# Kernel tuning notes

Measured on AMD Instinct MI355X. Metric: run time of the kernel, lower is better.

Reference implementation:

```python
import jax, jax.numpy as jnp
import numpy as np

WS = 7           # window size
N = WS * WS      # tokens per window = 49
C = 128          # embed dim
H = 4            # heads
HD = C // H      # head dim = 32
NW = 64          # num windows (mask leading dim)
B = 4096         # total windows = outer_batch * NW


def _relative_indexes():
    ch = np.arange(WS)
    cw = np.arange(WS)
    coords = np.stack(np.meshgrid(ch, cw, indexing='ij')).reshape(2, -1)  # [2, N]
    rel = coords[:, :, None] - coords[:, None, :]                          # [2, N, N]
    rel = rel.transpose(1, 2, 0)
    rel[:, :, 0] += WS - 1
    rel[:, :, 1] += WS - 1
    rel[:, :, 0] *= 2 * WS - 1
    return jnp.asarray(rel.sum(-1), dtype=jnp.int32)                       # [N, N]


def setup_inputs() -> dict:
    key = jax.random.key(0)
    ks = jax.random.split(key, 10)
    s = 0.02
    return {
        'query': jax.random.normal(ks[0], (B, N, C), jnp.float32),
        'source': jax.random.normal(ks[1], (B, N, C), jnp.float32),
        'mask': jnp.zeros((NW, N, N), jnp.float32),
        'q_w': jax.random.normal(ks[2], (C, C), jnp.float32) * s,
        'q_b': jnp.zeros((C,), jnp.float32),
        'kv_w': jax.random.normal(ks[3], (C, 2 * C), jnp.float32) * s,
        'kv_b': jnp.zeros((2 * C,), jnp.float32),
        'proj_w': jax.random.normal(ks[4], (C, C), jnp.float32) * s,
        'proj_b': jnp.zeros((C,), jnp.float32),
        'bias_table': jax.random.normal(ks[5], ((2 * WS - 1) ** 2, H), jnp.float32) * s,
        'rel_idx': _relative_indexes(),
    }


def reference(query, source, mask, q_w, q_b, kv_w, kv_b, proj_w, proj_b, bias_table, rel_idx):
    scale = HD ** -0.5
    q = query @ q_w + q_b                       # [B, N, C]
    kv = source @ kv_w + kv_b                   # [B, N, 2C]
    k, v = kv[..., :C], kv[..., C:]
    # [B, N, H, HD] -> [B, H, N, HD]
    q = q.reshape(B, N, H, HD).transpose(0, 2, 1, 3) * scale
    k = k.reshape(B, N, H, HD).transpose(0, 2, 1, 3)
    v = v.reshape(B, N, H, HD).transpose(0, 2, 1, 3)
    attn = jnp.einsum('bhnd,bhmd->bhnm', q, k)  # [B, H, N, N]
    # gathered relative positional bias: [1, H, N, N]
    bias = bias_table[rel_idx.reshape(-1)].reshape(N, N, H).transpose(2, 0, 1)[None]
    attn = attn + bias
    # mask: [NW, N, N] broadcast over outer batch and heads
    attn = attn.reshape(-1, NW, H, N, N) + mask[None, :, None]
    attn = attn.reshape(B, H, N, N)
    attn = jax.nn.softmax(attn, axis=-1)
    x = jnp.einsum('bhnm,bhmd->bnhd', attn, v).reshape(B, N, C)
    return x @ proj_w + proj_b
```

## Files before the change

kernel.cpp:

```cpp
#include <hip/hip_runtime.h>
#include <hip/hip_bf16.h>

#define NN 49
#define CC 128
#define HH 4
#define NWIN 64
#define BB 4096
#define QSCALE 0.17677669529663687f

typedef __attribute__((ext_vector_type(8))) short bf16x8;
typedef __attribute__((ext_vector_type(4))) float f32x4;
typedef unsigned short u16;
typedef unsigned int u32;

union U8 { u32 u[4]; bf16x8 v; };

__device__ __forceinline__ u16 f2b(float f) {
    __hip_bfloat16 h = __float2bfloat16(f);
    return __builtin_bit_cast(u16, h);
}
__device__ __forceinline__ float b2f(u16 u) { return __uint_as_float(((u32)u) << 16); }
__device__ __forceinline__ u32 cvtpk(float lo, float hi) {
    u32 r;
    asm("v_cvt_pk_bf16_f32 %0, %1, %2" : "=v"(r) : "v"(lo), "v"(hi));
    return r;
}
__device__ __forceinline__ uint2 pack4(float a, float b, float c, float d) {
    uint2 r;
    r.x = cvtpk(a, b);
    r.y = cvtpk(c, d);
    return r;
}
__device__ __forceinline__ f32x4 mfma16(bf16x8 a, bf16x8 b, f32x4 c) {
    return __builtin_amdgcn_mfma_f32_16x16x32_bf16(a, b, c, 0, 0, 0);
}
__device__ __forceinline__ char* adr256(u16* base, int row, int byte) {
    return (char*)base + row * 256 + (byte ^ ((row & 7) << 4));
}
__device__ __forceinline__ char* adr128(u16* base, int row, int byte) {
    return (char*)base + row * 128 + (byte ^ ((row & 7) << 4));
}

__global__ void prep_cbt(const float* __restrict__ bias_table, const int* __restrict__ rel_idx,
                         const float* __restrict__ mask, u16* __restrict__ cbt) {
    int idx = blockIdx.x * blockDim.x + threadIdx.x;
    int m = idx & 63, i = (idx >> 6) & 63, h = (idx >> 12) & 3, wv = idx >> 14;
    if (wv >= NWIN) return;
    float v = -1e9f;
    if (m < NN && i < NN)
        v = bias_table[rel_idx[i * NN + m] * HH + h] + mask[(wv * NN + i) * NN + m];
    cbt[idx] = f2b(v);
}

__global__ void prep_w(const float* __restrict__ qw, const float* __restrict__ qb,
                       const float* __restrict__ kvw, const float* __restrict__ pjw,
                       u16* __restrict__ qwp, u16* __restrict__ kvwp,
                       u16* __restrict__ pjwp, float* __restrict__ qbs) {
    int idx = blockIdx.x * blockDim.x + threadIdx.x;
    if (idx < 16384) {
        int i = idx & 7, lane = (idx >> 3) & 63, kt = (idx >> 9) & 3, nt = idx >> 11;
        int k = 32 * kt + 8 * (lane >> 4) + i, n = 16 * nt + (lane & 15);
        qwp[idx] = f2b(qw[k * CC + n] * QSCALE);
    } else if (idx < 49152) {
        int j = idx - 16384;
        int i = j & 7, lane = (j >> 3) & 63, kt = (j >> 9) & 3, nt = j >> 11;
        int k = 32 * kt + 8 * (lane >> 4) + i, n = 16 * nt + (lane & 15);
        kvwp[j] = f2b(kvw[k * 2 * CC + n]);
    } else if (idx < 65536) {
        int j = idx - 49152;
        int i = j & 7, lane = (j >> 3) & 63, kt = (j >> 9) & 3, nt = j >> 11;
        int k = 32 * kt + 8 * (lane >> 4) + i, n = 16 * nt + (lane & 15);
        pjwp[j] = f2b(pjw[k * CC + n]);
    } else if (idx < 65664) {
        int j = idx - 65536;
        qbs[j] = qb[j] * QSCALE;
    }
}

__global__ __launch_bounds__(512, 2)
void wmha_main(const float* __restrict__ query, const float* __restrict__ source,
               const u16* __restrict__ qwp, const u16* __restrict__ kvwp,
               const u16* __restrict__ pjwp, const float* __restrict__ qbs,
               const float* __restrict__ kv_b, const float* __restrict__ proj_b,
               const u16* __restrict__ cbt, float* __restrict__ out) {
    __shared__ u16 lds[40960];
    u16* SQ = lds;
    u16* SS = lds + 8192;
    u16* Qb = lds + 16384;
    u16* Kb = lds + 24576;
    u16* VT = lds + 32768;
    const int t = threadIdx.x;
    const int b = blockIdx.x;
    const int w = t >> 6, lane = t & 63;
    const int lq = lane & 15, qd = lane >> 4;
    const int mw = w >> 2;
    const int nw = w & 3;
    const int h = w >> 1;
    const int half = w & 1;

    {
        const int row = t >> 3, qu = t & 7;
        const size_t gbase = (size_t)b * NN * CC + row * CC + qu * 8;
        #pragma unroll
        for (int j = 0; j < 2; ++j) {
            U8 vq, vs;
            if (row < NN) {
                const float4* q4 = (const float4*)(query + gbase) + 16 * j;
                const float4* s4 = (const float4*)(source + gbase) + 16 * j;
                float4 a0 = q4[0], a1 = q4[1], c0 = s4[0], c1 = s4[1];
                vq.u[0] = cvtpk(a0.x, a0.y); vq.u[1] = cvtpk(a0.z, a0.w);
                vq.u[2] = cvtpk(a1.x, a1.y); vq.u[3] = cvtpk(a1.z, a1.w);
                vs.u[0] = cvtpk(c0.x, c0.y); vs.u[1] = cvtpk(c0.z, c0.w);
                vs.u[2] = cvtpk(c1.x, c1.y); vs.u[3] = cvtpk(c1.z, c1.w);
            } else {
                vq.u[0] = vq.u[1] = vq.u[2] = vq.u[3] = 0;
                vs.u[0] = vs.u[1] = vs.u[2] = vs.u[3] = 0;
            }
            *(bf16x8*)adr256(SQ, row, qu * 16 + 128 * j) = vq.v;
            *(bf16x8*)adr256(SS, row, qu * 16 + 128 * j) = vs.v;
        }
    }
    bf16x8 bwq[2][4];
    #pragma unroll
    for (int n2 = 0; n2 < 2; ++n2)
        #pragma unroll
        for (int kt = 0; kt < 4; ++kt)
            bwq[n2][kt] = *(const bf16x8*)(qwp + (((nw + 4 * n2) * 4 + kt) * 64 + lane) * 8);
    __syncthreads();

    {
        f32x4 acc[2][2] = {};
        #pragma unroll
        for (int m2 = 0; m2 < 2; ++m2) {
            bf16x8 a[4];
            #pragma unroll
            for (int kt = 0; kt < 4; ++kt)
                a[kt] = *(const bf16x8*)adr256(SQ, (2 * mw + m2) * 16 + lq, kt * 64 + qd * 16);
            __builtin_amdgcn_s_setprio(1);
            #pragma unroll
            for (int n2 = 0; n2 < 2; ++n2)
                #pragma unroll
                for (int kt = 0; kt < 4; ++kt)
                    acc[m2][n2] = mfma16(bwq[n2][kt], a[kt], acc[m2][n2]);
            __builtin_amdgcn_s_setprio(0);
        }
        #pragma unroll
        for (int n2 = 0; n2 < 2; ++n2) {
            const int cb0 = 16 * (nw + 4 * n2) + 4 * qd;
            const float4 bia = *(const float4*)(qbs + cb0);
            #pragma unroll
            for (int m2 = 0; m2 < 2; ++m2) {
                const int tok = (2 * mw + m2) * 16 + lq;
                uint2 pk = pack4(acc[m2][n2][0] + bia.x, acc[m2][n2][1] + bia.y,
                                 acc[m2][n2][2] + bia.z, acc[m2][n2][3] + bia.w);
                *(uint2*)adr256(Qb, tok, 2 * cb0) = pk;
            }
        }
    }
    {
        bf16x8 as[2][4];
        #pragma unroll
        for (int m2 = 0; m2 < 2; ++m2)
            #pragma unroll
            for (int kt = 0; kt < 4; ++kt)
                as[m2][kt] = *(const bf16x8*)adr256(SS, (2 * mw + m2) * 16 + lq, kt * 64 + qd * 16);
        {
            bf16x8 bwk[2][4];
            #pragma unroll
            for (int n2 = 0; n2 < 2; ++n2)
                #pragma unroll
                for (int kt = 0; kt < 4; ++kt)
                    bwk[n2][kt] = *(const bf16x8*)(kvwp + (((nw + 4 * n2) * 4 + kt) * 64 + lane) * 8);
            f32x4 acc[2][2] = {};
            __builtin_amdgcn_s_setprio(1);
            #pragma unroll
            for (int m2 = 0; m2 < 2; ++m2)
                #pragma unroll
                for (int n2 = 0; n2 < 2; ++n2)
                    #pragma unroll
                    for (int kt = 0; kt < 4; ++kt)
                        acc[m2][n2] = mfma16(bwk[n2][kt], as[m2][kt], acc[m2][n2]);
            __builtin_amdgcn_s_setprio(0);
            #pragma unroll
            for (int n2 = 0; n2 < 2; ++n2) {
                const int cb0 = 16 * (nw + 4 * n2) + 4 * qd;
                const float4 bia = *(const float4*)(kv_b + cb0);
                #pragma unroll
                for (int m2 = 0; m2 < 2; ++m2) {
                    const int tok = (2 * mw + m2) * 16 + lq;
                    uint2 pk = pack4(acc[m2][n2][0] + bia.x, acc[m2][n2][1] + bia.y,
                                     acc[m2][n2][2] + bia.z, acc[m2][n2][3] + bia.w);
                    *(uint2*)adr256(Kb, tok, 2 * cb0) = pk;
                }
            }
        }
        {
            bf16x8 bwv[2][4];
            #pragma unroll
            for (int n2 = 0; n2 < 2; ++n2)
                #pragma unroll
                for (int kt = 0; kt < 4; ++kt)
                    bwv[n2][kt] = *(const bf16x8*)(kvwp + (((8 + nw + 4 * n2) * 4 + kt) * 64 + lane) * 8);
            f32x4 acc[2][2] = {};
            __builtin_amdgcn_s_setprio(1);
            #pragma unroll
            for (int m2 = 0; m2 < 2; ++m2)
                #pragma unroll
                for (int n2 = 0; n2 < 2; ++n2)
                    #pragma unroll
                    for (int kt = 0; kt < 4; ++kt)
                        acc[m2][n2] = mfma16(as[m2][kt], bwv[n2][kt], acc[m2][n2]);
            __builtin_amdgcn_s_setprio(0);
            #pragma unroll
            for (int n2 = 0; n2 < 2; ++n2) {
                const int dim = 16 * (nw + 4 * n2) + lq;
                const float bias = kv_b[CC + dim];
                #pragma unroll
                for (int m2 = 0; m2 < 2; ++m2) {
                    uint2 pk = pack4(acc[m2][n2][0] + bias, acc[m2][n2][1] + bias,
                                     acc[m2][n2][2] + bias, acc[m2][n2][3] + bias);
                    *(uint2*)adr128(VT, dim, 2 * ((2 * mw + m2) * 16 + qd * 4)) = pk;
                }
            }
        }
    }
    __syncthreads();

    f32x4 s[2][4];
    bf16x8 vf[2][2];
    {
        bf16x8 kf[4], qf[2];
        #pragma unroll
        for (int a = 0; a < 4; ++a)
            kf[a] = *(const bf16x8*)adr256(Kb, a * 16 + lq, h * 64 + qd * 16);
        #pragma unroll
        for (int i = 0; i < 2; ++i)
            qf[i] = *(const bf16x8*)adr256(Qb, (2 * half + i) * 16 + lq, h * 64 + qd * 16);
        __builtin_amdgcn_s_setprio(1);
        #pragma unroll
        for (int i = 0; i < 2; ++i) {
            f32x4 z = {0.f, 0.f, 0.f, 0.f};
            #pragma unroll
            for (int a = 0; a < 4; ++a)
                s[i][a] = mfma16(kf[a], qf[i], z);
        }
        __builtin_amdgcn_s_setprio(0);
        #pragma unroll
        for (int dt = 0; dt < 2; ++dt)
            #pragma unroll
            for (int kt = 0; kt < 2; ++kt)
                vf[dt][kt] = *(const bf16x8*)adr128(VT, h * 32 + dt * 16 + lq, kt * 64 + qd * 16);
    }
    uint2 cbr[2][4];
    {
        const u16* cbb = cbt + ((size_t)((b & (NWIN - 1)) * HH + h) << 12);
        #pragma unroll
        for (int i = 0; i < 2; ++i)
            #pragma unroll
            for (int a = 0; a < 4; ++a)
                cbr[i][a] = *(const uint2*)(cbb + ((2 * half + i) * 16 + lq) * 64 + a * 16 + qd * 4);
    }
    __syncthreads();

    {
        u16* pb0 = Qb + w * 1024;
        u16* pb1 = Kb + w * 1024;
        float inv[2];
        #pragma unroll
        for (int i = 0; i < 2; ++i) {
            #pragma unroll
            for (int a = 0; a < 3; ++a) {
                s[i][a][0] += b2f((u16)(cbr[i][a].x & 0xffffu));
                s[i][a][1] += b2f((u16)(cbr[i][a].x >> 16));
                s[i][a][2] += b2f((u16)(cbr[i][a].y & 0xffffu));
                s[i][a][3] += b2f((u16)(cbr[i][a].y >> 16));
            }
            s[i][3][0] += b2f((u16)(cbr[i][3].x & 0xffffu));
            float m0 = s[i][3][0];
            #pragma unroll
            for (int a = 0; a < 3; ++a)
                #pragma unroll
                for (int r = 0; r < 4; ++r) m0 = fmaxf(m0, s[i][a][r]);
            m0 = fmaxf(m0, __shfl_xor(m0, 16));
            m0 = fmaxf(m0, __shfl_xor(m0, 32));
            uint2 pk[4];
            float sm = 0.f;
            #pragma unroll
            for (int a = 0; a < 3; ++a) {
                float p0 = __expf(s[i][a][0] - m0), p1 = __expf(s[i][a][1] - m0);
                float p2 = __expf(s[i][a][2] - m0), p3 = __expf(s[i][a][3] - m0);
                pk[a].x = cvtpk(p0, p1);
                pk[a].y = cvtpk(p2, p3);
                sm += (p0 + p1) + (p2 + p3);
            }
            float p30 = __expf(s[i][3][0] - m0);
            pk[3].x = cvtpk(p30, 0.f);
            pk[3].y = 0u;
            sm += p30;
            sm += __shfl_xor(sm, 16);
            sm += __shfl_xor(sm, 32);
            inv[i] = 1.f / sm;
            u16* pb = i ? pb1 : pb0;
            #pragma unroll
            for (int a = 0; a < 4; ++a)
                *(uint2*)adr128(pb, lq, 32 * a + 8 * qd) = pk[a];
        }
        asm volatile("s_waitcnt lgkmcnt(0)" ::: "memory");
        __builtin_amdgcn_sched_barrier(0);
        f32x4 o[2][2] = {};
        __builtin_amdgcn_s_setprio(1);
        #pragma unroll
        for (int kt = 0; kt < 2; ++kt) {
            bf16x8 pf0 = *(const bf16x8*)adr128(pb0, lq, 64 * kt + 16 * qd);
            bf16x8 pf1 = *(const bf16x8*)adr128(pb1, lq, 64 * kt + 16 * qd);
            #pragma unroll
            for (int dt = 0; dt < 2; ++dt) {
                o[0][dt] = mfma16(vf[dt][kt], pf0, o[0][dt]);
                o[1][dt] = mfma16(vf[dt][kt], pf1, o[1][dt]);
            }
        }
        __builtin_amdgcn_s_setprio(0);
        #pragma unroll
        for (int i = 0; i < 2; ++i)
            #pragma unroll
            for (int dt = 0; dt < 2; ++dt) {
                uint2 px = pack4(o[i][dt][0] * inv[i], o[i][dt][1] * inv[i],
                                 o[i][dt][2] * inv[i], o[i][dt][3] * inv[i]);
                *(uint2*)adr256(SQ, (2 * half + i) * 16 + lq, 64 * h + 32 * dt + 8 * qd) = px;
            }
    }

    {
        bf16x8 bw[2][4];
        #pragma unroll
        for (int n2 = 0; n2 < 2; ++n2)
            #pragma unroll
            for (int kt = 0; kt < 4; ++kt)
                bw[n2][kt] = *(const bf16x8*)(pjwp + (((nw + 4 * n2) * 4 + kt) * 64 + lane) * 8);
        __syncthreads();
        f32x4 acc[2][2] = {};
        #pragma unroll
        for (int m2 = 0; m2 < 2; ++m2) {
            bf16x8 a[4];
            #pragma unroll
            for (int kt = 0; kt < 4; ++kt)
                a[kt] = *(const bf16x8*)adr256(SQ, (2 * mw + m2) * 16 + lq, kt * 64 + qd * 16);
            __builtin_amdgcn_s_setprio(1);
            #pragma unroll
            for (int n2 = 0; n2 < 2; ++n2)
                #pragma unroll
                for (int kt = 0; kt < 4; ++kt)
                    acc[m2][n2] = mfma16(bw[n2][kt], a[kt], acc[m2][n2]);
            __builtin_amdgcn_s_setprio(0);
        }
        float* outb = out + (size_t)b * NN * CC;
        #pragma unroll
        for (int n2 = 0; n2 < 2; ++n2) {
            const int cb0 = 16 * (nw + 4 * n2) + 4 * qd;
            const float4 bia = *(const float4*)(proj_b + cb0);
            #pragma unroll
            for (int m2 = 0; m2 < 2; ++m2) {
                const int tok = (2 * mw + m2) * 16 + lq;
                if (tok < NN) {
                    float4 vst;
                    vst.x = acc[m2][n2][0] + bia.x;
                    vst.y = acc[m2][n2][1] + bia.y;
                    vst.z = acc[m2][n2][2] + bia.z;
                    vst.w = acc[m2][n2][3] + bia.w;
                    *(float4*)(outb + tok * CC + cb0) = vst;
                }
            }
        }
    }
}

extern "C" void kernel_launch(void* const* d_in, const int* in_sizes, int n_in,
                              void* d_out, int out_size, void* d_ws, size_t ws_size,
                              hipStream_t stream) {
    const float* query      = (const float*)d_in[0];
    const float* source     = (const float*)d_in[1];
    const float* mask       = (const float*)d_in[2];
    const float* q_w        = (const float*)d_in[3];
    const float* q_b        = (const float*)d_in[4];
    const float* kv_w       = (const float*)d_in[5];
    const float* kv_b       = (const float*)d_in[6];
    const float* proj_w     = (const float*)d_in[7];
    const float* proj_b     = (const float*)d_in[8];
    const float* bias_table = (const float*)d_in[9];
    const int*   rel_idx    = (const int*)d_in[10];
    float* out = (float*)d_out;

    u16* cbt   = (u16*)d_ws;
    u16* qwp   = cbt + 1048576;
    u16* kvwp  = qwp + 16384;
    u16* pjwp  = kvwp + 32768;
    float* qbs = (float*)(pjwp + 16384);

    prep_cbt<<<4096, 256, 0, stream>>>(bias_table, rel_idx, mask, cbt);
    prep_w<<<257, 256, 0, stream>>>(q_w, q_b, kv_w, proj_w, qwp, kvwp, pjwp, qbs);
    wmha_main<<<BB, 512, 0, stream>>>(query, source, qwp, kvwp, pjwp, qbs,
                                      kv_b, proj_b, cbt, out);
}
```

Measured before the change: 121.7 us.

## Alias LDS regions to shrink shared memory and raise occupancy

Shrinks per-block LDS from 80KB to 48KB by reusing three 16KB regions across phases (input staging, Q/K/V^T, probability buffers, attention output). It adds extra __syncthreads to guard the reuse, processes the two query tiles of P·V sequentially with a single probability buffer, and moves the V fragment loads later. Launch bounds now request 6 blocks per CU instead of 2, trading tighter register budgets and more barriers for more resident blocks to hide latency.

```diff
diff --git a/kernel.cpp b/kernel.cpp
--- a/kernel.cpp
+++ b/kernel.cpp
@@ -77,18 +77,16 @@
     }
 }
 
-__global__ __launch_bounds__(512, 2)
+__global__ __launch_bounds__(512, 6)
 void wmha_main(const float* __restrict__ query, const float* __restrict__ source,
                const u16* __restrict__ qwp, const u16* __restrict__ kvwp,
                const u16* __restrict__ pjwp, const float* __restrict__ qbs,
                const float* __restrict__ kv_b, const float* __restrict__ proj_b,
                const u16* __restrict__ cbt, float* __restrict__ out) {
-    __shared__ u16 lds[40960];
-    u16* SQ = lds;
-    u16* SS = lds + 8192;
-    u16* Qb = lds + 16384;
-    u16* Kb = lds + 24576;
-    u16* VT = lds + 32768;
+    __shared__ u16 lds[24576];
+    u16* R0 = lds;
+    u16* R1 = lds + 8192;
+    u16* R2 = lds + 16384;
     const int t = threadIdx.x;
     const int b = blockIdx.x;
     const int w = t >> 6, lane = t & 63;
@@ -116,8 +114,8 @@
                 vq.u[0] = vq.u[1] = vq.u[2] = vq.u[3] = 0;
                 vs.u[0] = vs.u[1] = vs.u[2] = vs.u[3] = 0;
             }
-            *(bf16x8*)adr256(SQ, row, qu * 16 + 128 * j) = vq.v;
-            *(bf16x8*)adr256(SS, row, qu * 16 + 128 * j) = vs.v;
+            *(bf16x8*)adr256(R0, row, qu * 16 + 128 * j) = vq.v;
+            *(bf16x8*)adr256(R2, row, qu * 16 + 128 * j) = vs.v;
         }
     }
     bf16x8 bwq[2][4];
@@ -135,7 +133,7 @@
             bf16x8 a[4];
             #pragma unroll
             for (int kt = 0; kt < 4; ++kt)
-                a[kt] = *(const bf16x8*)adr256(SQ, (2 * mw + m2) * 16 + lq, kt * 64 + qd * 16);
+                a[kt] = *(const bf16x8*)adr256(R0, (2 * mw + m2) * 16 + lq, kt * 64 + qd * 16);
             __builtin_amdgcn_s_setprio(1);
             #pragma unroll
             for (int n2 = 0; n2 < 2; ++n2)
@@ -153,17 +151,19 @@
                 const int tok = (2 * mw + m2) * 16 + lq;
                 uint2 pk = pack4(acc[m2][n2][0] + bia.x, acc[m2][n2][1] + bia.y,
                                  acc[m2][n2][2] + bia.z, acc[m2][n2][3] + bia.w);
-                *(uint2*)adr256(Qb, tok, 2 * cb0) = pk;
-            }
-        }
-    }
+                *(uint2*)adr256(R1, tok, 2 * cb0) = pk;
+            }
+        }
+    }
+    __syncthreads();
+
     {
         bf16x8 as[2][4];
         #pragma unroll
         for (int m2 = 0; m2 < 2; ++m2)
             #pragma unroll
             for (int kt = 0; kt < 4; ++kt)
-                as[m2][kt] = *(const bf16x8*)adr256(SS, (2 * mw + m2) * 16 + lq, kt * 64 + qd * 16);
+                as[m2][kt] = *(const bf16x8*)adr256(R2, (2 * mw + m2) * 16 + lq, kt * 64 + qd * 16);
         {
             bf16x8 bwk[2][4];
             #pragma unroll
@@ -190,7 +190,7 @@
                     const int tok = (2 * mw + m2) * 16 + lq;
                     uint2 pk = pack4(acc[m2][n2][0] + bia.x, acc[m2][n2][1] + bia.y,
                                      acc[m2][n2][2] + bia.z, acc[m2][n2][3] + bia.w);
-                    *(uint2*)adr256(Kb, tok, 2 * cb0) = pk;
+                    *(uint2*)adr256(R0, tok, 2 * cb0) = pk;
                 }
             }
         }
@@ -211,6 +211,7 @@
                     for (int kt = 0; kt < 4; ++kt)
                         acc[m2][n2] = mfma16(as[m2][kt], bwv[n2][kt], acc[m2][n2]);
             __builtin_amdgcn_s_setprio(0);
+            __syncthreads();
             #pragma unroll
             for (int n2 = 0; n2 < 2; ++n2) {
                 const int dim = 16 * (nw + 4 * n2) + lq;
@@ -219,23 +220,21 @@
                 for (int m2 = 0; m2 < 2; ++m2) {
                     uint2 pk = pack4(acc[m2][n2][0] + bias, acc[m2][n2][1] + bias,
                                      acc[m2][n2][2] + bias, acc[m2][n2][3] + bias);
-                    *(uint2*)adr128(VT, dim, 2 * ((2 * mw + m2) * 16 + qd * 4)) = pk;
+                    *(uint2*)adr128(R2, dim, 2 * ((2 * mw + m2) * 16 + qd * 4)) = pk;
                 }
             }
         }
     }
-    __syncthreads();
 
     f32x4 s[2][4];
-    bf16x8 vf[2][2];
     {
         bf16x8 kf[4], qf[2];
         #pragma unroll
         for (int a = 0; a < 4; ++a)
-            kf[a] = *(const bf16x8*)adr256(Kb, a * 16 + lq, h * 64 + qd * 16);
+            kf[a] = *(const bf16x8*)adr256(R0, a * 16 + lq, h * 64 + qd * 16);
         #pragma unroll
         for (int i = 0; i < 2; ++i)
-            qf[i] = *(const bf16x8*)adr256(Qb, (2 * half + i) * 16 + lq, h * 64 + qd * 16);
+            qf[i] = *(const bf16x8*)adr256(R1, (2 * half + i) * 16 + lq, h * 64 + qd * 16);
         __builtin_amdgcn_s_setprio(1);
         #pragma unroll
         for (int i = 0; i < 2; ++i) {
@@ -245,11 +244,6 @@
                 s[i][a] = mfma16(kf[a], qf[i], z);
         }
         __builtin_amdgcn_s_setprio(0);
-        #pragma unroll
-        for (int dt = 0; dt < 2; ++dt)
-            #pragma unroll
-            for (int kt = 0; kt < 2; ++kt)
-                vf[dt][kt] = *(const bf16x8*)adr128(VT, h * 32 + dt * 16 + lq, kt * 64 + qd * 16);
     }
     uint2 cbr[2][4];
     {
@@ -263,11 +257,16 @@
     __syncthreads();
 
     {
-        u16* pb0 = Qb + w * 1024;
-        u16* pb1 = Kb + w * 1024;
-        float inv[2];
+        bf16x8 vf[2][2];
+        #pragma unroll
+        for (int dt = 0; dt < 2; ++dt)
+            #pragma unroll
+            for (int kt = 0; kt < 2; ++kt)
+                vf[dt][kt] = *(const bf16x8*)adr128(R2, h * 32 + dt * 16 + lq, kt * 64 + qd * 16);
+        u16* pb = R0 + w * 1024;
         #pragma unroll
         for (int i = 0; i < 2; ++i) {
+            const int bq = 2 * half + i;
             #pragma unroll
             for (int a = 0; a < 3; ++a) {
                 s[i][a][0] += b2f((u16)(cbr[i][a].x & 0xffffu));
@@ -299,35 +298,30 @@
             sm += p30;
             sm += __shfl_xor(sm, 16);
             sm += __shfl_xor(sm, 32);
-            inv[i] = 1.f / sm;
-            u16* pb = i ? pb1 : pb0;
+            const float inv = 1.f / sm;
             #pragma unroll
             for (int a = 0; a < 4; ++a)
                 *(uint2*)adr128(pb, lq, 32 * a + 8 * qd) = pk[a];
-        }
-        asm volatile("s_waitcnt lgkmcnt(0)" ::: "memory");
-        __builtin_amdgcn_sched_barrier(0);
-        f32x4 o[2][2] = {};
-        __builtin_amdgcn_s_setprio(1);
-        #pragma unroll
-        for (int kt = 0; kt < 2; ++kt) {
-            bf16x8 pf0 = *(const bf16x8*)adr128(pb0, lq, 64 * kt + 16 * qd);
-            bf16x8 pf1 = *(const bf16x8*)adr128(pb1, lq, 64 * kt + 16 * qd);
+            asm volatile("s_waitcnt lgkmcnt(0)" ::: "memory");
+            __builtin_amdgcn_sched_barrier(0);
+            f32x4 o[2] = {{0.f,0.f,0.f,0.f},{0.f,0.f,0.f,0.f}};
+            __builtin_amdgcn_s_setprio(1);
+            #pragma unroll
+            for (int kt = 0; kt < 2; ++kt) {
+                bf16x8 pf = *(const bf16x8*)adr128(pb, lq, 64 * kt + 16 * qd);
+                #pragma unroll
+                for (int dt = 0; dt < 2; ++dt)
+                    o[dt] = mfma16(vf[dt][kt], pf, o[dt]);
+            }
+            __builtin_amdgcn_s_setprio(0);
+            __builtin_amdgcn_sched_barrier(0);
             #pragma unroll
             for (int dt = 0; dt < 2; ++dt) {
-                o[0][dt] = mfma16(vf[dt][kt], pf0, o[0][dt]);
-                o[1][dt] = mfma16(vf[dt][kt], pf1, o[1][dt]);
-            }
-        }
-        __builtin_amdgcn_s_setprio(0);
-        #pragma unroll
-        for (int i = 0; i < 2; ++i)
-            #pragma unroll
-            for (int dt = 0; dt < 2; ++dt) {
-                uint2 px = pack4(o[i][dt][0] * inv[i], o[i][dt][1] * inv[i],
-                                 o[i][dt][2] * inv[i], o[i][dt][3] * inv[i]);
-                *(uint2*)adr256(SQ, (2 * half + i) * 16 + lq, 64 * h + 32 * dt + 8 * qd) = px;
-            }
+                uint2 px = pack4(o[dt][0] * inv, o[dt][1] * inv,
+                                 o[dt][2] * inv, o[dt][3] * inv);
+                *(uint2*)adr256(R1, bq * 16 + lq, 64 * h + 32 * dt + 8 * qd) = px;
+            }
+        }
     }
 
     {
@@ -344,7 +338,7 @@
             bf16x8 a[4];
             #pragma unroll
             for (int kt = 0; kt < 4; ++kt)
-                a[kt] = *(const bf16x8*)adr256(SQ, (2 * mw + m2) * 16 + lq, kt * 64 + qd * 16);
+                a[kt] = *(const bf16x8*)adr256(R1, (2 * mw + m2) * 16 + lq, kt * 64 + qd * 16);
             __builtin_amdgcn_s_setprio(1);
             #pragma unroll
             for (int n2 = 0; n2 < 2; ++n2)
```

Result: slower. 208.6 us (+71.4%).

## Split fused window attention into QKV projection and attention/output kernels

Applied to the files above, without the earlier changes.

Splits the single fused kernel into two: one projects Q, K and V^T into swizzled bf16 images in workspace, the other loads those images and does attention plus the output projection. It falls back to the fused kernel when the workspace is too small. The likely aim is to cut per-kernel LDS and register pressure so occupancy or scheduling improves. The cost is an extra round trip of about 200MB of bf16 intermediates through global memory and one more launch.

```diff
diff --git a/kernel.cpp b/kernel.cpp
--- a/kernel.cpp
+++ b/kernel.cpp
@@ -78,6 +78,333 @@
 }
 
 __global__ __launch_bounds__(512, 2)
+void qkv_proj(const float* __restrict__ query, const float* __restrict__ source,
+              const u16* __restrict__ qwp, const u16* __restrict__ kvwp,
+              const float* __restrict__ qbs, const float* __restrict__ kv_b,
+              u16* __restrict__ qimg, u16* __restrict__ kimg, u16* __restrict__ vtimg) {
+    __shared__ u16 lds[16384];
+    u16* SQ = lds;
+    u16* SS = lds + 8192;
+    const int t = threadIdx.x;
+    const int b = blockIdx.x;
+    const int w = t >> 6, lane = t & 63;
+    const int lq = lane & 15, qd = lane >> 4;
+    const int mw = w >> 2, nw = w & 3;
+
+    {
+        const int row = t >> 3, qu = t & 7;
+        const size_t gbase = (size_t)b * NN * CC + row * CC + qu * 8;
+        #pragma unroll
+        for (int j = 0; j < 2; ++j) {
+            U8 vq, vs;
+            if (row < NN) {
+                const float4* q4 = (const float4*)(query + gbase) + 16 * j;
+                const float4* s4 = (const float4*)(source + gbase) + 16 * j;
+                float4 a0 = q4[0], a1 = q4[1], c0 = s4[0], c1 = s4[1];
+                vq.u[0] = cvtpk(a0.x, a0.y); vq.u[1] = cvtpk(a0.z, a0.w);
+                vq.u[2] = cvtpk(a1.x, a1.y); vq.u[3] = cvtpk(a1.z, a1.w);
+                vs.u[0] = cvtpk(c0.x, c0.y); vs.u[1] = cvtpk(c0.z, c0.w);
+                vs.u[2] = cvtpk(c1.x, c1.y); vs.u[3] = cvtpk(c1.z, c1.w);
+            } else {
+                vq.u[0] = vq.u[1] = vq.u[2] = vq.u[3] = 0;
+                vs.u[0] = vs.u[1] = vs.u[2] = vs.u[3] = 0;
+            }
+            *(bf16x8*)adr256(SQ, row, qu * 16 + 128 * j) = vq.v;
+            *(bf16x8*)adr256(SS, row, qu * 16 + 128 * j) = vs.v;
+        }
+    }
+    bf16x8 bwq[2][4];
+    #pragma unroll
+    for (int n2 = 0; n2 < 2; ++n2)
+        #pragma unroll
+        for (int kt = 0; kt < 4; ++kt)
+            bwq[n2][kt] = *(const bf16x8*)(qwp + (((nw + 4 * n2) * 4 + kt) * 64 + lane) * 8);
+    __syncthreads();
+
+    u16* qo  = qimg  + (size_t)b * 8192;
+    u16* ko  = kimg  + (size_t)b * 8192;
+    u16* vto = vtimg + (size_t)b * 8192;
+
+    {
+        f32x4 acc[2][2] = {};
+        #pragma unroll
+        for (int m2 = 0; m2 < 2; ++m2) {
+            bf16x8 a[4];
+            #pragma unroll
+            for (int kt = 0; kt < 4; ++kt)
+                a[kt] = *(const bf16x8*)adr256(SQ, (2 * mw + m2) * 16 + lq, kt * 64 + qd * 16);
+            __builtin_amdgcn_s_setprio(1);
+            #pragma unroll
+            for (int n2 = 0; n2 < 2; ++n2)
+                #pragma unroll
+                for (int kt = 0; kt < 4; ++kt)
+                    acc[m2][n2] = mfma16(bwq[n2][kt], a[kt], acc[m2][n2]);
+            __builtin_amdgcn_s_setprio(0);
+        }
+        #pragma unroll
+        for (int n2 = 0; n2 < 2; ++n2) {
+            const int cb0 = 16 * (nw + 4 * n2) + 4 * qd;
+            const float4 bia = *(const float4*)(qbs + cb0);
+            #pragma unroll
+            for (int m2 = 0; m2 < 2; ++m2) {
+                const int tok = (2 * mw + m2) * 16 + lq;
+                uint2 pk = pack4(acc[m2][n2][0] + bia.x, acc[m2][n2][1] + bia.y,
+                                 acc[m2][n2][2] + bia.z, acc[m2][n2][3] + bia.w);
+                *(uint2*)adr256(qo, tok, 2 * cb0) = pk;
+            }
+        }
+    }
+    {
+        bf16x8 as[2][4];
+        #pragma unroll
+        for (int m2 = 0; m2 < 2; ++m2)
+            #pragma unroll
+            for (int kt = 0; kt < 4; ++kt)
+                as[m2][kt] = *(const bf16x8*)adr256(SS, (2 * mw + m2) * 16 + lq, kt * 64 + qd * 16);
+        {
+            bf16x8 bwk[2][4];
+            #pragma unroll
+            for (int n2 = 0; n2 < 2; ++n2)
+                #pragma unroll
+                for (int kt = 0; kt < 4; ++kt)
+                    bwk[n2][kt] = *(const bf16x8*)(kvwp + (((nw + 4 * n2) * 4 + kt) * 64 + lane) * 8);
+            f32x4 acc[2][2] = {};
+            __builtin_amdgcn_s_setprio(1);
+            #pragma unroll
+            for (int m2 = 0; m2 < 2; ++m2)
+                #pragma unroll
+                for (int n2 = 0; n2 < 2; ++n2)
+                    #pragma unroll
+                    for (int kt = 0; kt < 4; ++kt)
+                        acc[m2][n2] = mfma16(bwk[n2][kt], as[m2][kt], acc[m2][n2]);
+            __builtin_amdgcn_s_setprio(0);
+            #pragma unroll
+            for (int n2 = 0; n2 < 2; ++n2) {
+                const int cb0 = 16 * (nw + 4 * n2) + 4 * qd;
+                const float4 bia = *(const float4*)(kv_b + cb0);
+                #pragma unroll
+                for (int m2 = 0; m2 < 2; ++m2) {
+                    const int tok = (2 * mw + m2) * 16 + lq;
+                    uint2 pk = pack4(acc[m2][n2][0] + bia.x, acc[m2][n2][1] + bia.y,
+                                     acc[m2][n2][2] + bia.z, acc[m2][n2][3] + bia.w);
+                    *(uint2*)adr256(ko, tok, 2 * cb0) = pk;
+                }
+            }
+        }
+        {
+            bf16x8 bwv[2][4];
+            #pragma unroll
+            for (int n2 = 0; n2 < 2; ++n2)
+                #pragma unroll
+                for (int kt = 0; kt < 4; ++kt)
+                    bwv[n2][kt] = *(const bf16x8*)(kvwp + (((8 + nw + 4 * n2) * 4 + kt) * 64 + lane) * 8);
+            f32x4 acc[2][2] = {};
+            __builtin_amdgcn_s_setprio(1);
+            #pragma unroll
+            for (int m2 = 0; m2 < 2; ++m2)
+                #pragma unroll
+                for (int n2 = 0; n2 < 2; ++n2)
+                    #pragma unroll
+                    for (int kt = 0; kt < 4; ++kt)
+                        acc[m2][n2] = mfma16(as[m2][kt], bwv[n2][kt], acc[m2][n2]);
+            __builtin_amdgcn_s_setprio(0);
+            #pragma unroll
+            for (int n2 = 0; n2 < 2; ++n2) {
+                const int dim = 16 * (nw + 4 * n2) + lq;
+                const float bias = kv_b[CC + dim];
+                #pragma unroll
+                for (int m2 = 0; m2 < 2; ++m2) {
+                    uint2 pk = pack4(acc[m2][n2][0] + bias, acc[m2][n2][1] + bias,
+                                     acc[m2][n2][2] + bias, acc[m2][n2][3] + bias);
+                    *(uint2*)adr128(vto, dim, 2 * ((2 * mw + m2) * 16 + qd * 4)) = pk;
+                }
+            }
+        }
+    }
+}
+
+__global__ __launch_bounds__(512, 2)
+void attn_out(const u16* __restrict__ qimg, const u16* __restrict__ kimg,
+              const u16* __restrict__ vtimg, const u16* __restrict__ pjwp,
+              const float* __restrict__ proj_b, const u16* __restrict__ cbt,
+              float* __restrict__ out) {
+    __shared__ u16 lds[24576];
+    u16* Qi = lds;
+    u16* Ki = lds + 8192;
+    u16* VTi = lds + 16384;
+    const int t = threadIdx.x;
+    const int b = blockIdx.x;
+    const int w = t >> 6, lane = t & 63;
+    const int lq = lane & 15, qd = lane >> 4;
+    const int mw = w >> 2, nw = w & 3;
+    const int h = w >> 1, half = w & 1;
+
+    {
+        const u16* gq = qimg  + (size_t)b * 8192;
+        const u16* gk = kimg  + (size_t)b * 8192;
+        const u16* gv = vtimg + (size_t)b * 8192;
+        #pragma unroll
+        for (int j = 0; j < 2; ++j) {
+            const int off = (t + j * 512) * 8;
+            uint4 a = *(const uint4*)(gq + off);
+            uint4 c = *(const uint4*)(gk + off);
+            uint4 d = *(const uint4*)(gv + off);
+            *(uint4*)(Qi + off) = a;
+            *(uint4*)(Ki + off) = c;
+            *(uint4*)(VTi + off) = d;
+        }
+    }
+    __syncthreads();
+
+    f32x4 s[2][4];
+    bf16x8 vf[2][2];
+    {
+        bf16x8 kf[4], qf[2];
+        #pragma unroll
+        for (int a = 0; a < 4; ++a)
+            kf[a] = *(const bf16x8*)adr256(Ki, a * 16 + lq, h * 64 + qd * 16);
+        #pragma unroll
+        for (int i = 0; i < 2; ++i)
+            qf[i] = *(const bf16x8*)adr256(Qi, (2 * half + i) * 16 + lq, h * 64 + qd * 16);
+        __builtin_amdgcn_s_setprio(1);
+        #pragma unroll
+        for (int i = 0; i < 2; ++i) {
+            f32x4 z = {0.f, 0.f, 0.f, 0.f};
+            #pragma unroll
+            for (int a = 0; a < 4; ++a)
+                s[i][a] = mfma16(kf[a], qf[i], z);
+        }
+        __builtin_amdgcn_s_setprio(0);
+        #pragma unroll
+        for (int dt = 0; dt < 2; ++dt)
+            #pragma unroll
+            for (int kt = 0; kt < 2; ++kt)
+                vf[dt][kt] = *(const bf16x8*)adr128(VTi, h * 32 + dt * 16 + lq, kt * 64 + qd * 16);
+    }
+    uint2 cbr[2][4];
+    {
+        const u16* cbb = cbt + ((size_t)((b & (NWIN - 1)) * HH + h) << 12);
+        #pragma unroll
+        for (int i = 0; i < 2; ++i)
+            #pragma unroll
+            for (int a = 0; a < 4; ++a)
+                cbr[i][a] = *(const uint2*)(cbb + ((2 * half + i) * 16 + lq) * 64 + a * 16 + qd * 4);
+    }
+    __syncthreads();
+
+    {
+        u16* pb0 = Qi + w * 1024;
+        u16* pb1 = Ki + w * 1024;
+        float inv[2];
+        #pragma unroll
+        for (int i = 0; i < 2; ++i) {
+            #pragma unroll
+            for (int a = 0; a < 3; ++a) {
+                s[i][a][0] += b2f((u16)(cbr[i][a].x & 0xffffu));
+                s[i][a][1] += b2f((u16)(cbr[i][a].x >> 16));
+                s[i][a][2] += b2f((u16)(cbr[i][a].y & 0xffffu));
+                s[i][a][3] += b2f((u16)(cbr[i][a].y >> 16));
+            }
+            s[i][3][0] += b2f((u16)(cbr[i][3].x & 0xffffu));
+            float m0 = s[i][3][0];
+            #pragma unroll
+            for (int a = 0; a < 3; ++a)
+                #pragma unroll
+                for (int r = 0; r < 4; ++r) m0 = fmaxf(m0, s[i][a][r]);
+            m0 = fmaxf(m0, __shfl_xor(m0, 16));
+            m0 = fmaxf(m0, __shfl_xor(m0, 32));
+            uint2 pk[4];
+            float sm = 0.f;
+            #pragma unroll
+            for (int a = 0; a < 3; ++a) {
+                float p0 = __expf(s[i][a][0] - m0), p1 = __expf(s[i][a][1] - m0);
+                float p2 = __expf(s[i][a][2] - m0), p3 = __expf(s[i][a][3] - m0);
+                pk[a].x = cvtpk(p0, p1);
+                pk[a].y = cvtpk(p2, p3);
+                sm += (p0 + p1) + (p2 + p3);
+            }
+            float p30 = __expf(s[i][3][0] - m0);
+            pk[3].x = cvtpk(p30, 0.f);
+            pk[3].y = 0u;
+            sm += p30;
+            sm += __shfl_xor(sm, 16);
+            sm += __shfl_xor(sm, 32);
+            inv[i] = 1.f / sm;
+            u16* pb = i ? pb1 : pb0;
+            #pragma unroll
+            for (int a = 0; a < 4; ++a)
+                *(uint2*)adr128(pb, lq, 32 * a + 8 * qd) = pk[a];
+        }
+        asm volatile("s_waitcnt lgkmcnt(0)" ::: "memory");
+        __builtin_amdgcn_sched_barrier(0);
+        f32x4 o[2][2] = {};
+        __builtin_amdgcn_s_setprio(1);
+        #pragma unroll
+        for (int kt = 0; kt < 2; ++kt) {
+            bf16x8 pf0 = *(const bf16x8*)adr128(pb0, lq, 64 * kt + 16 * qd);
+            bf16x8 pf1 = *(const bf16x8*)adr128(pb1, lq, 64 * kt + 16 * qd);
+            #pragma unroll
+            for (int dt = 0; dt < 2; ++dt) {
+                o[0][dt] = mfma16(vf[dt][kt], pf0, o[0][dt]);
+                o[1][dt] = mfma16(vf[dt][kt], pf1, o[1][dt]);
+            }
+        }
+        __builtin_amdgcn_s_setprio(0);
+        #pragma unroll
+        for (int i = 0; i < 2; ++i)
+            #pragma unroll
+            for (int dt = 0; dt < 2; ++dt) {
+                uint2 px = pack4(o[i][dt][0] * inv[i], o[i][dt][1] * inv[i],
+                                 o[i][dt][2] * inv[i], o[i][dt][3] * inv[i]);
+                *(uint2*)adr256(VTi, (2 * half + i) * 16 + lq, 64 * h + 32 * dt + 8 * qd) = px;
+            }
+    }
+
+    {
+        bf16x8 bw[2][4];
+        #pragma unroll
+        for (int n2 = 0; n2 < 2; ++n2)
+            #pragma unroll
+            for (int kt = 0; kt < 4; ++kt)
+                bw[n2][kt] = *(const bf16x8*)(pjwp + (((nw + 4 * n2) * 4 + kt) * 64 + lane) * 8);
+        __syncthreads();
+        f32x4 acc[2][2] = {};
+        #pragma unroll
+        for (int m2 = 0; m2 < 2; ++m2) {
+            bf16x8 a[4];
+            #pragma unroll
+            for (int kt = 0; kt < 4; ++kt)
+                a[kt] = *(const bf16x8*)adr256(VTi, (2 * mw + m2) * 16 + lq, kt * 64 + qd * 16);
+            __builtin_amdgcn_s_setprio(1);
+            #pragma unroll
+            for (int n2 = 0; n2 < 2; ++n2)
+                #pragma unroll
+                for (int kt = 0; kt < 4; ++kt)
+                    acc[m2][n2] = mfma16(bw[n2][kt], a[kt], acc[m2][n2]);
+            __builtin_amdgcn_s_setprio(0);
+        }
+        float* outb = out + (size_t)b * NN * CC;
+        #pragma unroll
+        for (int n2 = 0; n2 < 2; ++n2) {
+            const int cb0 = 16 * (nw + 4 * n2) + 4 * qd;
+            const float4 bia = *(const float4*)(proj_b + cb0);
+            #pragma unroll
+            for (int m2 = 0; m2 < 2; ++m2) {
+                const int tok = (2 * mw + m2) * 16 + lq;
+                if (tok < NN) {
+                    float4 vst;
+                    vst.x = acc[m2][n2][0] + bia.x;
+                    vst.y = acc[m2][n2][1] + bia.y;
+                    vst.z = acc[m2][n2][2] + bia.z;
+                    vst.w = acc[m2][n2][3] + bia.w;
+                    *(float4*)(outb + tok * CC + cb0) = vst;
+                }
+            }
+        }
+    }
+}
+
+__global__ __launch_bounds__(512, 2)
 void wmha_main(const float* __restrict__ query, const float* __restrict__ source,
                const u16* __restrict__ qwp, const u16* __restrict__ kvwp,
                const u16* __restrict__ pjwp, const float* __restrict__ qbs,
@@ -93,10 +420,8 @@
     const int b = blockIdx.x;
     const int w = t >> 6, lane = t & 63;
     const int lq = lane & 15, qd = lane >> 4;
-    const int mw = w >> 2;
-    const int nw = w & 3;
-    const int h = w >> 1;
-    const int half = w & 1;
+    const int mw = w >> 2, nw = w & 3;
+    const int h = w >> 1, half = w & 1;
 
     {
         const int row = t >> 3, qu = t & 7;
@@ -395,9 +720,19 @@
     u16* kvwp  = qwp + 16384;
     u16* pjwp  = kvwp + 32768;
     float* qbs = (float*)(pjwp + 16384);
+    u16* qimg  = (u16*)(qbs + 128);
+    u16* kimg  = qimg + (size_t)BB * 8192;
+    u16* vtimg = kimg + (size_t)BB * 8192;
+    const size_t need = (size_t)((char*)(vtimg + (size_t)BB * 8192) - (char*)d_ws);
 
     prep_cbt<<<4096, 256, 0, stream>>>(bias_table, rel_idx, mask, cbt);
     prep_w<<<257, 256, 0, stream>>>(q_w, q_b, kv_w, proj_w, qwp, kvwp, pjwp, qbs);
-    wmha_main<<<BB, 512, 0, stream>>>(query, source, qwp, kvwp, pjwp, qbs,
-                                      kv_b, proj_b, cbt, out);
-}
+    if (ws_size >= need) {
+        qkv_proj<<<BB, 512, 0, stream>>>(query, source, qwp, kvwp, qbs, kv_b,
+                                         qimg, kimg, vtimg);
+        attn_out<<<BB, 512, 0, stream>>>(qimg, kimg, vtimg, pjwp, proj_b, cbt, out);
+    } else {
+        wmha_main<<<BB, 512, 0, stream>>>(query, source, qwp, kvwp, pjwp, qbs,
+                                          kv_b, proj_b, cbt, out);
+    }
+}
```

Result: slower. 195.8 us (+60.9%).
